# Kernel tuning notes

Measured on AMD Instinct MI355X. Metric: run time of the kernel, lower is better.

Reference implementation:

```python
import jax, jax.numpy as jnp
import numpy as np

GRID_SIZE = 5
SPLINE_ORDER = 3
GRID_RANGE = (-1.0, 1.0)
EPS = 1e-8


def _make_grid():
    h = (GRID_RANGE[1] - GRID_RANGE[0]) / GRID_SIZE
    # knots: [-spline_order, ..., grid_size + spline_order] * h + lo  -> 12 values
    return jnp.arange(-SPLINE_ORDER, GRID_SIZE + SPLINE_ORDER + 1, dtype=jnp.float32) * h + GRID_RANGE[0]


def _bspline_basis(x, grid):
    # x: [N, in]  ->  bases: [N, in, num_basis] with num_basis = grid_size + spline_order
    xe = x[..., None]                                   # [N, in, 1]
    bases = ((xe >= grid[:-1]) & (xe < grid[1:])).astype(x.dtype)  # [N, in, 11]
    for k in range(1, SPLINE_ORDER + 1):
        left = (xe - grid[: -(k + 1)]) / (grid[k:-1] - grid[: -(k + 1)] + EPS) * bases[..., :-1]
        right = (grid[k + 1:] - xe) / (grid[k + 1:] - grid[1:-k] + EPS) * bases[..., 1:]
        bases = left + right
    return bases                                        # [N, in, 8]


def setup_inputs() -> dict:
    key = jax.random.key(0)
    k1, k2, k3 = jax.random.split(key, 3)
    in_f, out_f, num_basis = 1024, 1024, GRID_SIZE + SPLINE_ORDER
    N = 4096
    x = jax.random.normal(k1, (N, in_f), dtype=jnp.float32)
    base_weight = jax.random.normal(k2, (out_f, in_f), dtype=jnp.float32) * (1.0 / np.sqrt(in_f))
    base_bias = jnp.zeros((out_f,), dtype=jnp.float32)
    spline_weight = jax.random.normal(k3, (out_f, in_f, num_basis), dtype=jnp.float32) * (1.0 / np.sqrt(in_f))
    return {"x": x, "base_weight": base_weight, "base_bias": base_bias, "spline_weight": spline_weight}


def reference(x, base_weight, base_bias, spline_weight):
    grid = _make_grid()
    # base path: SiLU(x) @ W_base^T + b
    base_out = jax.nn.silu(x) @ base_weight.T + base_bias          # [N, out]
    # spline path: Cox-de Boor basis then contraction over (in, basis)
    basis = _bspline_basis(x, grid)                                 # [N, in, 8]
    spline_out = jnp.einsum('nib,oib->no', basis, spline_weight)    # [N, out]
    return base_out + spline_out
```

## Files before the change

kernel.cpp:

```cpp
#include <hip/hip_runtime.h>
#include <hip/hip_bf16.h>
#include <stdint.h>

#define IN_F 1024
#define OUT_F 1024
#define NB 8
#define KDIM (IN_F + IN_F * NB)
#define NROWS 4096
#define SLICE_ELEMS (NROWS * OUT_F)
#define PREP_BLOCKS ((NROWS * IN_F) / 256)
#define WCONV_BLOCKS ((OUT_F * KDIM) / (4 * 256))

typedef __attribute__((ext_vector_type(8))) short bf16x8;
typedef __attribute__((ext_vector_type(4))) short bf16x4;
typedef __attribute__((ext_vector_type(4))) float f32x4;

__device__ __forceinline__ void bspline8(float x, float b8[8]) {
  float u = (x + 2.2f) * 2.5f;
  bool in = (u >= 0.0f) && (u < 11.0f);
  float uc = fminf(fmaxf(u, 0.0f), 10.99f);
  int i = (int)uc;
  float f = uc - (float)i;
  float g = 1.0f - f;
  float f2 = f * f, f3 = f2 * f;
  const float s = 1.0f / 6.0f;
  float v0 = f3 * s;
  float v1 = (-3.0f * f3 + 3.0f * f2 + 3.0f * f + 1.0f) * s;
  float v2 = (3.0f * f3 - 6.0f * f2 + 4.0f) * s;
  float v3 = g * g * g * s;
#pragma unroll
  for (int j = 0; j < 8; ++j) {
    int d = i - j;
    float r = (d == 0) ? v0 : (d == 1) ? v1 : (d == 2) ? v2 : (d == 3) ? v3 : 0.0f;
    b8[j] = in ? r : 0.0f;
  }
}

__global__ void prep_all_kernel(const float* __restrict__ x, const float* __restrict__ bw,
                                const float* __restrict__ sw, __hip_bfloat16* __restrict__ A,
                                __hip_bfloat16* __restrict__ W) {
  if (blockIdx.x < PREP_BLOCKS) {
    int idx = blockIdx.x * 256 + threadIdx.x;
    int n = idx >> 10;
    int i = idx & 1023;
    float xv = x[idx];
    float sl = xv / (1.0f + __expf(-xv));
    __hip_bfloat16* row = A + (size_t)n * KDIM;
    row[i] = __float2bfloat16(sl);
    float b8[8];
    bspline8(xv, b8);
    alignas(16) __hip_bfloat16 tmp[8];
#pragma unroll
    for (int c = 0; c < 8; ++c) tmp[c] = __float2bfloat16(b8[c]);
    *(bf16x8*)(row + IN_F + i * 8) = *(const bf16x8*)tmp;
  } else {
    int v = (blockIdx.x - PREP_BLOCKS) * 256 + threadIdx.x;
    int e = v * 4;
    int o = e / KDIM;
    int k = e - o * KDIM;
    float4 val = (k < IN_F) ? *(const float4*)(bw + o * IN_F + k)
                            : *(const float4*)(sw + (size_t)o * (IN_F * NB) + (k - IN_F));
    alignas(8) __hip_bfloat16 t[4];
    t[0] = __float2bfloat16(val.x);
    t[1] = __float2bfloat16(val.y);
    t[2] = __float2bfloat16(val.z);
    t[3] = __float2bfloat16(val.w);
    *(bf16x4*)(W + e) = *(const bf16x4*)t;
  }
}

__global__ __launch_bounds__(256) void gemm_kernel(const __hip_bfloat16* __restrict__ A,
                                                   const __hip_bfloat16* __restrict__ W,
                                                   float* __restrict__ dst,
                                                   const float* __restrict__ bias,
                                                   int kslice, int use_bias) {
  __shared__ __hip_bfloat16 lA[2][128 * 64];
  __shared__ __hip_bfloat16 lB[2][128 * 64];
  const int tid = threadIdx.x;
  const int wave = tid >> 6;
  const int lane = tid & 63;
  const int bm = blockIdx.x * 128;
  const int bn = blockIdx.y * 128;
  const int z = blockIdx.z;
  float* __restrict__ d = dst + (size_t)z * SLICE_ELEMS;
  const int kbeg = z * kslice;
  const int iters = kslice / 64;
  const int srow = lane & 15;
  const int skc = (lane >> 4) * 8;
  const int wm = (wave & 1) * 64;
  const int wn = (wave >> 1) * 64;
  const int r = lane & 15;
  const int quad = lane >> 4;

  const int g0 = wave * 2;
  const __hip_bfloat16* gA[2];
  const __hip_bfloat16* gB[2];
  gA[0] = A + (size_t)(bm + g0 * 16 + srow) * KDIM + kbeg + skc;
  gA[1] = gA[0] + (size_t)16 * KDIM;
  gB[0] = W + (size_t)(bn + g0 * 16 + srow) * KDIM + kbeg + skc;
  gB[1] = gB[0] + (size_t)16 * KDIM;

  f32x4 acc[4][4];
#pragma unroll
  for (int a = 0; a < 4; ++a)
#pragma unroll
    for (int b = 0; b < 4; ++b) acc[a][b] = (f32x4){0.f, 0.f, 0.f, 0.f};

#define STAGE(IT, BUF)                                                                             \
  do {                                                                                             \
    const int koff = (IT) * 64;                                                                    \
    _Pragma("unroll") for (int h = 0; h < 2; ++h) {                                                \
      _Pragma("unroll") for (int s = 0; s < 2; ++s) {                                              \
        const __hip_bfloat16* srcA = gA[h] + koff + s * 32;                                        \
        const __hip_bfloat16* srcB = gB[h] + koff + s * 32;                                        \
        __hip_bfloat16* dA = &lA[BUF][((g0 + h) * 2 + s) * 512];                                   \
        __hip_bfloat16* dB = &lB[BUF][((g0 + h) * 2 + s) * 512];                                   \
        __builtin_amdgcn_global_load_lds((const __attribute__((address_space(1))) void*)srcA,      \
                                         (__attribute__((address_space(3))) void*)dA, 16, 0, 0);   \
        __builtin_amdgcn_global_load_lds((const __attribute__((address_space(1))) void*)srcB,      \
                                         (__attribute__((address_space(3))) void*)dB, 16, 0, 0);   \
      }                                                                                            \
    }                                                                                              \
  } while (0)

  STAGE(0, 0);
  __syncthreads();

  for (int it = 0; it < iters; ++it) {
    const int p = it & 1;
    if (it + 1 < iters) STAGE(it + 1, p ^ 1);

#pragma unroll
    for (int s = 0; s < 2; ++s) {
      bf16x8 af[4], bfr[4];
#pragma unroll
      for (int t = 0; t < 4; ++t) {
        af[t] = *(const bf16x8*)&lA[p][(((wm >> 4) + t) * 2 + s) * 512 + lane * 8];
        bfr[t] = *(const bf16x8*)&lB[p][(((wn >> 4) + t) * 2 + s) * 512 + lane * 8];
      }
#pragma unroll
      for (int tm = 0; tm < 4; ++tm)
#pragma unroll
        for (int tn = 0; tn < 4; ++tn)
          acc[tm][tn] =
              __builtin_amdgcn_mfma_f32_16x16x32_bf16(af[tm], bfr[tn], acc[tm][tn], 0, 0, 0);
    }

    __syncthreads();
  }
#undef STAGE

#pragma unroll
  for (int tm = 0; tm < 4; ++tm) {
#pragma unroll
    for (int tn = 0; tn < 4; ++tn) {
      const int col = bn + wn + tn * 16 + r;
      const float bv = use_bias ? bias[col] : 0.0f;
#pragma unroll
      for (int reg = 0; reg < 4; ++reg) {
        const int rowi = bm + wm + tm * 16 + quad * 4 + reg;
        d[(size_t)rowi * OUT_F + col] = acc[tm][tn][reg] + bv;
      }
    }
  }
}

__global__ void reduce_kernel(const float* __restrict__ P, const float* __restrict__ bias,
                              float* __restrict__ out, int S) {
  int v = blockIdx.x * 256 + threadIdx.x;
  int e = v * 4;
  int o = e & (OUT_F - 1);
  float4 acc = *(const float4*)(bias + o);
  for (int s = 0; s < S; ++s) {
    float4 p = *(const float4*)(P + (size_t)s * SLICE_ELEMS + e);
    acc.x += p.x;
    acc.y += p.y;
    acc.z += p.z;
    acc.w += p.w;
  }
  *(float4*)(out + e) = acc;
}

__global__ void kan_fallback(const float* __restrict__ x, const float* __restrict__ bw,
                             const float* __restrict__ bb, const float* __restrict__ sw,
                             float* __restrict__ out) {
  __shared__ float act[KDIM];
  int n = blockIdx.x;
  for (int i = threadIdx.x; i < IN_F; i += 256) {
    float xv = x[(size_t)n * IN_F + i];
    act[i] = xv / (1.0f + __expf(-xv));
    float b8[8];
    bspline8(xv, b8);
#pragma unroll
    for (int c = 0; c < 8; ++c) act[IN_F + i * 8 + c] = b8[c];
  }
  __syncthreads();
  for (int o = threadIdx.x; o < OUT_F; o += 256) {
    float s = bb[o];
    const float* wbp = bw + (size_t)o * IN_F;
    for (int k = 0; k < IN_F; ++k) s += act[k] * wbp[k];
    const float* wsp = sw + (size_t)o * (IN_F * NB);
    for (int k = 0; k < IN_F * NB; ++k) s += act[IN_F + k] * wsp[k];
    out[(size_t)n * OUT_F + o] = s;
  }
}

extern "C" void kernel_launch(void* const* d_in, const int* in_sizes, int n_in, void* d_out,
                              int out_size, void* d_ws, size_t ws_size, hipStream_t stream) {
  const float* x = (const float*)d_in[0];
  const float* bw = (const float*)d_in[1];
  const float* bb = (const float*)d_in[2];
  const float* sw = (const float*)d_in[3];
  float* out = (float*)d_out;

  const size_t needA = (size_t)NROWS * KDIM * 2;
  const size_t needW = (size_t)OUT_F * KDIM * 2;
  const size_t sliceB = (size_t)SLICE_ELEMS * 4;
  if (ws_size < needA + needW) {
    kan_fallback<<<NROWS, 256, 0, stream>>>(x, bw, bb, sw, out);
    return;
  }
  __hip_bfloat16* A = (__hip_bfloat16*)d_ws;
  __hip_bfloat16* W = (__hip_bfloat16*)((char*)d_ws + needA);
  float* P = (float*)((char*)d_ws + needA + needW);
  const size_t avail = ws_size - needA - needW;
  int S = (avail >= 2 * sliceB) ? 2 : 1;

  prep_all_kernel<<<PREP_BLOCKS + WCONV_BLOCKS, 256, 0, stream>>>(x, bw, sw, A, W);
  if (S == 1) {
    gemm_kernel<<<dim3(NROWS / 128, OUT_F / 128, 1), 256, 0, stream>>>(A, W, out, bb, KDIM, 1);
  } else {
    gemm_kernel<<<dim3(NROWS / 128, OUT_F / 128, S), 256, 0, stream>>>(A, W, P, bb, KDIM / S, 0);
    reduce_kernel<<<SLICE_ELEMS / (4 * 256), 256, 0, stream>>>(P, bb, out, S);
  }
}
```

Before: 257.9 us.

## Replace GEMM with 256x256 8-wave ping-pong pipelined kernel and 4-way split-K

Replaces the 128x128, 4-wave GEMM with a 256x256 tile kernel that uses 8 waves. The K loop is split into fine-grained phases that interleave half-tile global-to-LDS loads with MFMA quads, using explicit barriers, waitcnt and setprio to overlap memory and compute. Split-K grows to 4 slices when the workspace allows, so the launch still has enough blocks. The larger tile raises data reuse per block but adds LDS and register pressure, and the extra split slices add reduction traffic.

After: 219.4 us. 1.18x faster.

```diff
diff --git a/kernel.cpp b/kernel.cpp
--- a/kernel.cpp
+++ b/kernel.cpp
@@ -69,96 +69,200 @@
   }
 }
 
-__global__ __launch_bounds__(256) void gemm_kernel(const __hip_bfloat16* __restrict__ A,
-                                                   const __hip_bfloat16* __restrict__ W,
-                                                   float* __restrict__ dst,
-                                                   const float* __restrict__ bias,
-                                                   int kslice, int use_bias) {
-  __shared__ __hip_bfloat16 lA[2][128 * 64];
-  __shared__ __hip_bfloat16 lB[2][128 * 64];
+__global__ __launch_bounds__(512, 2) void gemm8_kernel(const __hip_bfloat16* __restrict__ A,
+                                                       const __hip_bfloat16* __restrict__ W,
+                                                       float* __restrict__ dst,
+                                                       const float* __restrict__ bias,
+                                                       int kslice, int use_bias) {
+  __shared__ __hip_bfloat16 lA[2][16384];
+  __shared__ __hip_bfloat16 lB[2][16384];
   const int tid = threadIdx.x;
   const int wave = tid >> 6;
   const int lane = tid & 63;
-  const int bm = blockIdx.x * 128;
-  const int bn = blockIdx.y * 128;
+  const int warp_m = wave >> 2;
+  const int warp_n = wave & 3;
+  const int bm = blockIdx.x * 256;
+  const int bn = blockIdx.y * 256;
   const int z = blockIdx.z;
   float* __restrict__ d = dst + (size_t)z * SLICE_ELEMS;
   const int kbeg = z * kslice;
-  const int iters = kslice / 64;
+  const int NT = kslice >> 6;
+  const int NIT = NT >> 1;
   const int srow = lane & 15;
   const int skc = (lane >> 4) * 8;
-  const int wm = (wave & 1) * 64;
-  const int wn = (wave >> 1) * 64;
   const int r = lane & 15;
   const int quad = lane >> 4;
 
-  const int g0 = wave * 2;
-  const __hip_bfloat16* gA[2];
-  const __hip_bfloat16* gB[2];
-  gA[0] = A + (size_t)(bm + g0 * 16 + srow) * KDIM + kbeg + skc;
-  gA[1] = gA[0] + (size_t)16 * KDIM;
-  gB[0] = W + (size_t)(bn + g0 * 16 + srow) * KDIM + kbeg + skc;
-  gB[1] = gB[0] + (size_t)16 * KDIM;
-
-  f32x4 acc[4][4];
-#pragma unroll
-  for (int a = 0; a < 4; ++a)
+  const __hip_bfloat16* rowA[2];
+  const __hip_bfloat16* rowB[2];
+  rowA[0] = A + (size_t)(bm + (0 * 8 + wave) * 16 + srow) * KDIM + kbeg + skc;
+  rowA[1] = A + (size_t)(bm + (1 * 8 + wave) * 16 + srow) * KDIM + kbeg + skc;
+  rowB[0] = W + (size_t)(bn + (0 * 8 + wave) * 16 + srow) * KDIM + kbeg + skc;
+  rowB[1] = W + (size_t)(bn + (1 * 8 + wave) * 16 + srow) * KDIM + kbeg + skc;
+
+  f32x4 acc[8][4];
+#pragma unroll
+  for (int a = 0; a < 8; ++a)
 #pragma unroll
     for (int b = 0; b < 4; ++b) acc[a][b] = (f32x4){0.f, 0.f, 0.f, 0.f};
 
-#define STAGE(IT, BUF)                                                                             \
-  do {                                                                                             \
-    const int koff = (IT) * 64;                                                                    \
-    _Pragma("unroll") for (int h = 0; h < 2; ++h) {                                                \
-      _Pragma("unroll") for (int s = 0; s < 2; ++s) {                                              \
-        const __hip_bfloat16* srcA = gA[h] + koff + s * 32;                                        \
-        const __hip_bfloat16* srcB = gB[h] + koff + s * 32;                                        \
-        __hip_bfloat16* dA = &lA[BUF][((g0 + h) * 2 + s) * 512];                                   \
-        __hip_bfloat16* dB = &lB[BUF][((g0 + h) * 2 + s) * 512];                                   \
-        __builtin_amdgcn_global_load_lds((const __attribute__((address_space(1))) void*)srcA,      \
-                                         (__attribute__((address_space(3))) void*)dA, 16, 0, 0);   \
-        __builtin_amdgcn_global_load_lds((const __attribute__((address_space(1))) void*)srcB,      \
-                                         (__attribute__((address_space(3))) void*)dB, 16, 0, 0);   \
-      }                                                                                            \
-    }                                                                                              \
-  } while (0)
-
-  STAGE(0, 0);
-  __syncthreads();
-
-  for (int it = 0; it < iters; ++it) {
-    const int p = it & 1;
-    if (it + 1 < iters) STAGE(it + 1, p ^ 1);
-
-#pragma unroll
-    for (int s = 0; s < 2; ++s) {
-      bf16x8 af[4], bfr[4];
-#pragma unroll
-      for (int t = 0; t < 4; ++t) {
-        af[t] = *(const bf16x8*)&lA[p][(((wm >> 4) + t) * 2 + s) * 512 + lane * 8];
-        bfr[t] = *(const bf16x8*)&lB[p][(((wn >> 4) + t) * 2 + s) * 512 + lane * 8];
-      }
-#pragma unroll
-      for (int tm = 0; tm < 4; ++tm)
-#pragma unroll
-        for (int tn = 0; tn < 4; ++tn)
-          acc[tm][tn] =
-              __builtin_amdgcn_mfma_f32_16x16x32_bf16(af[tm], bfr[tn], acc[tm][tn], 0, 0, 0);
-    }
-
-    __syncthreads();
-  }
-#undef STAGE
-
-#pragma unroll
-  for (int tm = 0; tm < 4; ++tm) {
+#define GLOAD(SRC, DST)                                                                      \
+  __builtin_amdgcn_global_load_lds((const __attribute__((address_space(1))) void*)(SRC),     \
+                                   (__attribute__((address_space(3))) void*)(DST), 16, 0, 0)
+
+#define STAGE_HALF(TILE, HID, SLOT)                                              \
+  do {                                                                           \
+    const int tu_ = (TILE);                                                      \
+    const int ts_ = tu_ < NT ? tu_ : NT - 1;                                     \
+    if ((HID) < 2) {                                                             \
+      const __hip_bfloat16* s_ = rowA[(HID)] + (size_t)ts_ * 64;                 \
+      __hip_bfloat16* d_ = &lA[(SLOT)][(((HID) * 8 + wave) * 2 + 0) * 512];      \
+      GLOAD(s_, d_);                                                             \
+      GLOAD(s_ + 32, d_ + 512);                                                  \
+    } else {                                                                     \
+      const __hip_bfloat16* s_ = rowB[(HID) - 2] + (size_t)ts_ * 64;             \
+      __hip_bfloat16* d_ = &lB[(SLOT)][((((HID) - 2) * 8 + wave) * 2 + 0) * 512];\
+      GLOAD(s_, d_);                                                             \
+      GLOAD(s_ + 32, d_ + 512);                                                  \
+    }                                                                            \
+  } while (0)
+
+  bf16x8 a03[4][2], a47[4][2], bfr[4][2];
+
+#define LOAD_A03(SLOT)                                                                      \
+  do {                                                                                      \
+    _Pragma("unroll") for (int t = 0; t < 4; ++t) {                                         \
+      a03[t][0] = *(const bf16x8*)&lA[(SLOT)][((warp_m * 8 + t) * 2 + 0) * 512 + lane * 8]; \
+      a03[t][1] = *(const bf16x8*)&lA[(SLOT)][((warp_m * 8 + t) * 2 + 1) * 512 + lane * 8]; \
+    }                                                                                       \
+  } while (0)
+#define LOAD_A47(SLOT)                                                                          \
+  do {                                                                                          \
+    _Pragma("unroll") for (int t = 0; t < 4; ++t) {                                             \
+      a47[t][0] = *(const bf16x8*)&lA[(SLOT)][((warp_m * 8 + 4 + t) * 2 + 0) * 512 + lane * 8]; \
+      a47[t][1] = *(const bf16x8*)&lA[(SLOT)][((warp_m * 8 + 4 + t) * 2 + 1) * 512 + lane * 8]; \
+    }                                                                                           \
+  } while (0)
+#define LOAD_B(SLOT)                                                                        \
+  do {                                                                                      \
+    _Pragma("unroll") for (int u = 0; u < 4; ++u) {                                         \
+      bfr[u][0] = *(const bf16x8*)&lB[(SLOT)][((warp_n * 4 + u) * 2 + 0) * 512 + lane * 8]; \
+      bfr[u][1] = *(const bf16x8*)&lB[(SLOT)][((warp_n * 4 + u) * 2 + 1) * 512 + lane * 8]; \
+    }                                                                                       \
+  } while (0)
+
+#define MFMA_QUAD(AF, TM0, TN0)                                                              \
+  do {                                                                                       \
+    _Pragma("unroll") for (int tm = 0; tm < 4; ++tm)                                         \
+    _Pragma("unroll") for (int tn = 0; tn < 2; ++tn)                                         \
+    _Pragma("unroll") for (int s = 0; s < 2; ++s)                                            \
+        acc[(TM0) + tm][(TN0) + tn] = __builtin_amdgcn_mfma_f32_16x16x32_bf16(               \
+            AF[tm][s], bfr[(TN0) + tn][s], acc[(TM0) + tm][(TN0) + tn], 0, 0, 0);            \
+  } while (0)
+
+#define PH_BAR_LGKM()                                        \
+  do {                                                       \
+    __builtin_amdgcn_s_barrier();                            \
+    asm volatile("s_waitcnt lgkmcnt(0)" ::: "memory");       \
+    __builtin_amdgcn_sched_barrier(0);                       \
+  } while (0)
+#define PH_BAR()                                             \
+  do {                                                       \
+    __builtin_amdgcn_s_barrier();                            \
+    __builtin_amdgcn_sched_barrier(0);                       \
+  } while (0)
+#define PH_END()                                             \
+  do {                                                       \
+    __builtin_amdgcn_s_setprio(0);                           \
+    __builtin_amdgcn_sched_barrier(0);                       \
+    __builtin_amdgcn_s_barrier();                            \
+  } while (0)
+
+  STAGE_HALF(0, 2, 0);
+  STAGE_HALF(0, 3, 0);
+  STAGE_HALF(0, 0, 0);
+  STAGE_HALF(0, 1, 0);
+  STAGE_HALF(1, 2, 1);
+  STAGE_HALF(1, 3, 1);
+  STAGE_HALF(1, 0, 1);
+  asm volatile("s_waitcnt vmcnt(6)" ::: "memory");
+  __builtin_amdgcn_sched_barrier(0);
+  __builtin_amdgcn_s_barrier();
+
+  for (int i = 0; i < NIT; ++i) {
+    const int t2 = 2 * i + 2, t3 = 2 * i + 3;
+    LOAD_A03(0);
+    LOAD_B(0);
+    STAGE_HALF(2 * i + 1, 1, 1);
+    PH_BAR_LGKM();
+    __builtin_amdgcn_s_setprio(1);
+    MFMA_QUAD(a03, 0, 0);
+    PH_END();
+    LOAD_A47(0);
+    STAGE_HALF(t2, 2, 0);
+    PH_BAR_LGKM();
+    __builtin_amdgcn_s_setprio(1);
+    MFMA_QUAD(a47, 4, 0);
+    PH_END();
+    STAGE_HALF(t2, 3, 0);
+    PH_BAR();
+    __builtin_amdgcn_s_setprio(1);
+    MFMA_QUAD(a03, 0, 2);
+    PH_END();
+    STAGE_HALF(t2, 0, 0);
+    asm volatile("s_waitcnt vmcnt(6)" ::: "memory");
+    __builtin_amdgcn_sched_barrier(0);
+    PH_BAR();
+    __builtin_amdgcn_s_setprio(1);
+    MFMA_QUAD(a47, 4, 2);
+    PH_END();
+    LOAD_A03(1);
+    LOAD_B(1);
+    STAGE_HALF(t2, 1, 0);
+    PH_BAR_LGKM();
+    __builtin_amdgcn_s_setprio(1);
+    MFMA_QUAD(a03, 0, 0);
+    PH_END();
+    LOAD_A47(1);
+    STAGE_HALF(t3, 2, 1);
+    PH_BAR_LGKM();
+    __builtin_amdgcn_s_setprio(1);
+    MFMA_QUAD(a47, 4, 0);
+    PH_END();
+    STAGE_HALF(t3, 3, 1);
+    PH_BAR();
+    __builtin_amdgcn_s_setprio(1);
+    MFMA_QUAD(a03, 0, 2);
+    PH_END();
+    STAGE_HALF(t3, 0, 1);
+    asm volatile("s_waitcnt vmcnt(6)" ::: "memory");
+    __builtin_amdgcn_sched_barrier(0);
+    PH_BAR();
+    __builtin_amdgcn_s_setprio(1);
+    MFMA_QUAD(a47, 4, 2);
+    PH_END();
+  }
+  asm volatile("s_waitcnt vmcnt(0)" ::: "memory");
+
+#undef STAGE_HALF
+#undef GLOAD
+#undef LOAD_A03
+#undef LOAD_A47
+#undef LOAD_B
+#undef MFMA_QUAD
+#undef PH_BAR_LGKM
+#undef PH_BAR
+#undef PH_END
+
+#pragma unroll
+  for (int tm = 0; tm < 8; ++tm) {
 #pragma unroll
     for (int tn = 0; tn < 4; ++tn) {
-      const int col = bn + wn + tn * 16 + r;
+      const int col = bn + warp_n * 64 + tn * 16 + r;
       const float bv = use_bias ? bias[col] : 0.0f;
 #pragma unroll
       for (int reg = 0; reg < 4; ++reg) {
-        const int rowi = bm + wm + tm * 16 + quad * 4 + reg;
+        const int rowi = bm + warp_m * 128 + tm * 16 + quad * 4 + reg;
         d[(size_t)rowi * OUT_F + col] = acc[tm][tn][reg] + bv;
       }
     }
@@ -224,13 +328,13 @@
   __hip_bfloat16* W = (__hip_bfloat16*)((char*)d_ws + needA);
   float* P = (float*)((char*)d_ws + needA + needW);
   const size_t avail = ws_size - needA - needW;
-  int S = (avail >= 2 * sliceB) ? 2 : 1;
+  int S = (avail >= 4 * sliceB) ? 4 : (avail >= 2 * sliceB) ? 2 : 1;
 
   prep_all_kernel<<<PREP_BLOCKS + WCONV_BLOCKS, 256, 0, stream>>>(x, bw, sw, A, W);
   if (S == 1) {
-    gemm_kernel<<<dim3(NROWS / 128, OUT_F / 128, 1), 256, 0, stream>>>(A, W, out, bb, KDIM, 1);
+    gemm8_kernel<<<dim3(NROWS / 256, OUT_F / 256, 1), 512, 0, stream>>>(A, W, out, bb, KDIM, 1);
   } else {
-    gemm_kernel<<<dim3(NROWS / 128, OUT_F / 128, S), 256, 0, stream>>>(A, W, P, bb, KDIM / S, 0);
+    gemm8_kernel<<<dim3(NROWS / 256, OUT_F / 256, S), 512, 0, stream>>>(A, W, P, bb, KDIM / S, 0);
     reduce_kernel<<<SLICE_ELEMS / (4 * 256), 256, 0, stream>>>(P, bb, out, S);
   }
 }
```

## Use 256x256 GEMM tile with triple-buffered LDS pipeline and 4-way split-K

Applied to the files above, without the earlier changes.

Replaces the 128x128, 4-wave GEMM with a 256x256, 8-wave kernel. Each wave computes a 128x64 sub-tile, so every LDS fragment feeds more MFMAs. K steps of 32 are staged through a three-slot LDS ring using direct global-to-LDS loads. A operand registers are double-buffered, with explicit waitcnt, sched_barrier and setprio around the MFMA block to overlap loads with compute. Split-K is raised to 4 slices when workspace allows, to keep enough blocks in flight with the larger tile. The cost is more partial-sum traffic in the reduce kernel and heavy register and LDS use per block.

Result: faster. 222.7 us (-13.6%).

```diff
diff --git a/kernel.cpp b/kernel.cpp
--- a/kernel.cpp
+++ b/kernel.cpp
@@ -69,96 +69,137 @@
   }
 }
 
-__global__ __launch_bounds__(256) void gemm_kernel(const __hip_bfloat16* __restrict__ A,
-                                                   const __hip_bfloat16* __restrict__ W,
-                                                   float* __restrict__ dst,
-                                                   const float* __restrict__ bias,
-                                                   int kslice, int use_bias) {
-  __shared__ __hip_bfloat16 lA[2][128 * 64];
-  __shared__ __hip_bfloat16 lB[2][128 * 64];
+__global__ __launch_bounds__(512, 2) void gemm10_kernel(const __hip_bfloat16* __restrict__ A,
+                                                        const __hip_bfloat16* __restrict__ W,
+                                                        float* __restrict__ dst,
+                                                        const float* __restrict__ bias,
+                                                        int kslice, int use_bias) {
+  __shared__ __hip_bfloat16 lA[3][8192];
+  __shared__ __hip_bfloat16 lB[3][8192];
   const int tid = threadIdx.x;
   const int wave = tid >> 6;
   const int lane = tid & 63;
-  const int bm = blockIdx.x * 128;
-  const int bn = blockIdx.y * 128;
+  const int warp_m = wave >> 2;
+  const int warp_n = wave & 3;
+  const int bm = blockIdx.x * 256;
+  const int bn = blockIdx.y * 256;
   const int z = blockIdx.z;
+
   float* __restrict__ d = dst + (size_t)z * SLICE_ELEMS;
   const int kbeg = z * kslice;
-  const int iters = kslice / 64;
+  const int NT = kslice >> 5;
   const int srow = lane & 15;
   const int skc = (lane >> 4) * 8;
-  const int wm = (wave & 1) * 64;
-  const int wn = (wave >> 1) * 64;
   const int r = lane & 15;
   const int quad = lane >> 4;
 
-  const int g0 = wave * 2;
-  const __hip_bfloat16* gA[2];
-  const __hip_bfloat16* gB[2];
-  gA[0] = A + (size_t)(bm + g0 * 16 + srow) * KDIM + kbeg + skc;
-  gA[1] = gA[0] + (size_t)16 * KDIM;
-  gB[0] = W + (size_t)(bn + g0 * 16 + srow) * KDIM + kbeg + skc;
-  gB[1] = gB[0] + (size_t)16 * KDIM;
-
-  f32x4 acc[4][4];
-#pragma unroll
-  for (int a = 0; a < 4; ++a)
+  const __hip_bfloat16* rowA[2];
+  const __hip_bfloat16* rowB[2];
+  rowA[0] = A + (size_t)(bm + (0 * 8 + wave) * 16 + srow) * KDIM + kbeg + skc;
+  rowA[1] = A + (size_t)(bm + (1 * 8 + wave) * 16 + srow) * KDIM + kbeg + skc;
+  rowB[0] = W + (size_t)(bn + (0 * 8 + wave) * 16 + srow) * KDIM + kbeg + skc;
+  rowB[1] = W + (size_t)(bn + (1 * 8 + wave) * 16 + srow) * KDIM + kbeg + skc;
+
+  f32x4 acc[8][4];
+#pragma unroll
+  for (int a = 0; a < 8; ++a)
 #pragma unroll
     for (int b = 0; b < 4; ++b) acc[a][b] = (f32x4){0.f, 0.f, 0.f, 0.f};
 
-#define STAGE(IT, BUF)                                                                             \
-  do {                                                                                             \
-    const int koff = (IT) * 64;                                                                    \
-    _Pragma("unroll") for (int h = 0; h < 2; ++h) {                                                \
-      _Pragma("unroll") for (int s = 0; s < 2; ++s) {                                              \
-        const __hip_bfloat16* srcA = gA[h] + koff + s * 32;                                        \
-        const __hip_bfloat16* srcB = gB[h] + koff + s * 32;                                        \
-        __hip_bfloat16* dA = &lA[BUF][((g0 + h) * 2 + s) * 512];                                   \
-        __hip_bfloat16* dB = &lB[BUF][((g0 + h) * 2 + s) * 512];                                   \
-        __builtin_amdgcn_global_load_lds((const __attribute__((address_space(1))) void*)srcA,      \
-                                         (__attribute__((address_space(3))) void*)dA, 16, 0, 0);   \
-        __builtin_amdgcn_global_load_lds((const __attribute__((address_space(1))) void*)srcB,      \
-                                         (__attribute__((address_space(3))) void*)dB, 16, 0, 0);   \
-      }                                                                                            \
-    }                                                                                              \
-  } while (0)
-
-  STAGE(0, 0);
-  __syncthreads();
-
-  for (int it = 0; it < iters; ++it) {
-    const int p = it & 1;
-    if (it + 1 < iters) STAGE(it + 1, p ^ 1);
-
-#pragma unroll
-    for (int s = 0; s < 2; ++s) {
-      bf16x8 af[4], bfr[4];
-#pragma unroll
-      for (int t = 0; t < 4; ++t) {
-        af[t] = *(const bf16x8*)&lA[p][(((wm >> 4) + t) * 2 + s) * 512 + lane * 8];
-        bfr[t] = *(const bf16x8*)&lB[p][(((wn >> 4) + t) * 2 + s) * 512 + lane * 8];
-      }
-#pragma unroll
-      for (int tm = 0; tm < 4; ++tm)
-#pragma unroll
-        for (int tn = 0; tn < 4; ++tn)
-          acc[tm][tn] =
-              __builtin_amdgcn_mfma_f32_16x16x32_bf16(af[tm], bfr[tn], acc[tm][tn], 0, 0, 0);
-    }
-
-    __syncthreads();
-  }
-#undef STAGE
-
-#pragma unroll
-  for (int tm = 0; tm < 4; ++tm) {
+#define GLOAD(SRC, DST)                                                                      \
+  __builtin_amdgcn_global_load_lds((const __attribute__((address_space(1))) void*)(SRC),     \
+                                   (__attribute__((address_space(3))) void*)(DST), 16, 0, 0)
+
+#define STAGE_TILE(TILE, SLOT)                                            \
+  do {                                                                    \
+    const int tu_ = (TILE);                                               \
+    const int ts_ = tu_ < NT ? tu_ : NT - 1;                              \
+    const size_t ko_ = (size_t)ts_ * 32;                                  \
+    GLOAD(rowA[0] + ko_, &lA[(SLOT)][(0 * 8 + wave) * 512]);              \
+    GLOAD(rowA[1] + ko_, &lA[(SLOT)][(1 * 8 + wave) * 512]);              \
+    GLOAD(rowB[0] + ko_, &lB[(SLOT)][(0 * 8 + wave) * 512]);              \
+    GLOAD(rowB[1] + ko_, &lB[(SLOT)][(1 * 8 + wave) * 512]);              \
+  } while (0)
+
+  bf16x8 a0[8], a1[8], bfr[4];
+
+#define LOAD_A(DST, SLOT)                                                        \
+  do {                                                                           \
+    _Pragma("unroll") for (int t = 0; t < 8; ++t)                                \
+        DST[t] = *(const bf16x8*)&lA[(SLOT)][(warp_m * 8 + t) * 512 + lane * 8]; \
+  } while (0)
+#define LOAD_B(SLOT)                                                             \
+  do {                                                                           \
+    _Pragma("unroll") for (int u = 0; u < 4; ++u)                                \
+        bfr[u] = *(const bf16x8*)&lB[(SLOT)][(warp_n * 4 + u) * 512 + lane * 8]; \
+  } while (0)
+
+#define MFMA_ALL(ACUR)                                                                       \
+  do {                                                                                       \
+    _Pragma("unroll") for (int tm = 0; tm < 8; ++tm)                                         \
+    _Pragma("unroll") for (int tn = 0; tn < 4; ++tn)                                         \
+        acc[tm][tn] =                                                                        \
+            __builtin_amdgcn_mfma_f32_16x16x32_bf16(ACUR[tm], bfr[tn], acc[tm][tn], 0, 0, 0);\
+  } while (0)
+
+#define PIN() __builtin_amdgcn_sched_barrier(0)
+
+#define TILE_BODY(T, SLN, SLS, ACUR, ANXT)                   \
+  do {                                                       \
+    LOAD_A(ANXT, SLN);    \
+    STAGE_TILE((T) + 3, SLS);                                \
+    PIN();                                                   \
+    __builtin_amdgcn_s_setprio(1);                           \
+    MFMA_ALL(ACUR); \
+    __builtin_amdgcn_s_setprio(0);                           \
+    PIN();                                                   \
+    LOAD_B(SLN);                \
+    asm volatile("s_waitcnt lgkmcnt(0)" ::: "memory");       \
+    PIN();                                                   \
+    asm volatile("s_waitcnt vmcnt(4)" ::: "memory");         \
+    PIN();                                                   \
+    __builtin_amdgcn_s_barrier();                            \
+  } while (0)
+
+  STAGE_TILE(0, 0);
+  STAGE_TILE(1, 1);
+  STAGE_TILE(2, 2);
+  asm volatile("s_waitcnt vmcnt(4)" ::: "memory");
+  PIN();
+  __builtin_amdgcn_s_barrier();
+  LOAD_A(a0, 0);
+  LOAD_B(0);
+  PIN();
+
+  const int nit = NT / 6;
+  for (int i = 0; i < nit; ++i) {
+    const int b = 6 * i;
+    TILE_BODY(b + 0, 1, 0, a0, a1);
+    TILE_BODY(b + 1, 2, 1, a1, a0);
+    TILE_BODY(b + 2, 0, 2, a0, a1);
+    TILE_BODY(b + 3, 1, 0, a1, a0);
+    TILE_BODY(b + 4, 2, 1, a0, a1);
+    TILE_BODY(b + 5, 0, 2, a1, a0);
+  }
+  asm volatile("s_waitcnt vmcnt(0)" ::: "memory");
+
+#undef TILE_BODY
+#undef STAGE_TILE
+#undef GLOAD
+#undef LOAD_A
+#undef LOAD_B
+#undef MFMA_ALL
+#undef PIN
+
+#pragma unroll
+  for (int tm = 0; tm < 8; ++tm) {
 #pragma unroll
     for (int tn = 0; tn < 4; ++tn) {
-      const int col = bn + wn + tn * 16 + r;
+      const int col = bn + warp_n * 64 + tn * 16 + r;
       const float bv = use_bias ? bias[col] : 0.0f;
 #pragma unroll
       for (int reg = 0; reg < 4; ++reg) {
-        const int rowi = bm + wm + tm * 16 + quad * 4 + reg;
+        const int rowi = bm + warp_m * 128 + tm * 16 + quad * 4 + reg;
         d[(size_t)rowi * OUT_F + col] = acc[tm][tn][reg] + bv;
       }
     }
@@ -224,13 +265,13 @@
   __hip_bfloat16* W = (__hip_bfloat16*)((char*)d_ws + needA);
   float* P = (float*)((char*)d_ws + needA + needW);
   const size_t avail = ws_size - needA - needW;
-  int S = (avail >= 2 * sliceB) ? 2 : 1;
+  int S = (avail >= 4 * sliceB) ? 4 : (avail >= 2 * sliceB) ? 2 : 1;
 
   prep_all_kernel<<<PREP_BLOCKS + WCONV_BLOCKS, 256, 0, stream>>>(x, bw, sw, A, W);
   if (S == 1) {
-    gemm_kernel<<<dim3(NROWS / 128, OUT_F / 128, 1), 256, 0, stream>>>(A, W, out, bb, KDIM, 1);
+    gemm10_kernel<<<dim3(NROWS / 256, OUT_F / 256, 1), 512, 0, stream>>>(A, W, out, bb, KDIM, 1);
   } else {
-    gemm_kernel<<<dim3(NROWS / 128, OUT_F / 128, S), 256, 0, stream>>>(A, W, P, bb, KDIM / S, 0);
+    gemm10_kernel<<<dim3(NROWS / 256, OUT_F / 256, S), 512, 0, stream>>>(A, W, P, bb, KDIM / S, 0);
     reduce_kernel<<<SLICE_ELEMS / (4 * 256), 256, 0, stream>>>(P, bb, out, S);
   }
 }
```
